# Performance work log

Hardware: AMD Instinct MI355X
Metric: run time of the kernel (lower is better)

The kernel has to match this reference:

```python
import jax, jax.numpy as jnp
import numpy as np

BETA = 0.2        # RPE learning rate (init kwarg, unused in forward output math except P update)
THRESH = 0.5      # BrainCog IFNode default firing threshold; v starts at 0 -> spike = (x >= THRESH)
N_NEURONS = 33554432


def setup_inputs() -> dict:
    key = jax.random.key(0)
    spikes = jax.random.uniform(key, (N_NEURONS,), dtype=jnp.float32)
    P = jnp.zeros((N_NEURONS,), dtype=jnp.float32)  # reward prediction state
    return {"spikes": spikes, "P": P}


def reference(spikes, P):
    # Vectorized IF neurons: membrane v = 0 + spikes; fire if v >= threshold (hard reset).
    out_spikes = (spikes >= THRESH).astype(spikes.dtype)   # [n_neurons]
    S = out_spikes.mean()                                  # scalar mean firing rate
    delta = S - P                                          # [n_neurons] reward prediction error
    # (State update in original: P <- P + BETA * delta; forward returns (delta, out_spikes).)
    return (delta, out_spikes)
```

## Files before the change

kernel.cpp:

```cpp
#include <hip/hip_runtime.h>


#define THRESH 0.5f
#define BLOCK  256
#define GRID   2048

typedef float v4f __attribute__((ext_vector_type(4)));

__device__ __forceinline__ int spike4(const v4f s, v4f& o) {
    o.x = (s.x >= THRESH) ? 1.0f : 0.0f;
    o.y = (s.y >= THRESH) ? 1.0f : 0.0f;
    o.z = (s.z >= THRESH) ? 1.0f : 0.0f;
    o.w = (s.w >= THRESH) ? 1.0f : 0.0f;
    return (int)o.x + (int)o.y + (int)o.z + (int)o.w;
}

__global__ __launch_bounds__(BLOCK) void spike_count_kernel(
    const v4f* __restrict__ spikes4,
    v4f* __restrict__ out_spikes4,
    unsigned int* __restrict__ partials,
    int n4, int chunk)
{
    const int tid   = threadIdx.x;
    const int start = blockIdx.x * chunk;
    const int end   = min(start + chunk, n4);
    int cnt = 0;

    int i = start + tid;
    for (; i + 3 * BLOCK < end; i += 4 * BLOCK) {
        v4f a = spikes4[i];
        v4f b = spikes4[i +     BLOCK];
        v4f c = spikes4[i + 2 * BLOCK];
        v4f d = spikes4[i + 3 * BLOCK];
        v4f oa, ob, oc, od;
        cnt += spike4(a, oa);
        cnt += spike4(b, ob);
        cnt += spike4(c, oc);
        cnt += spike4(d, od);
        out_spikes4[i]             = oa;
        out_spikes4[i +     BLOCK] = ob;
        out_spikes4[i + 2 * BLOCK] = oc;
        out_spikes4[i + 3 * BLOCK] = od;
    }
    for (; i < end; i += BLOCK) {
        v4f s = spikes4[i];
        v4f o;
        cnt += spike4(s, o);
        out_spikes4[i] = o;
    }

    #pragma unroll
    for (int off = 32; off > 0; off >>= 1)
        cnt += __shfl_down(cnt, off, 64);

    __shared__ int wave_sums[BLOCK / 64];
    const int lane = tid & 63;
    const int wid  = tid >> 6;
    if (lane == 0) wave_sums[wid] = cnt;
    __syncthreads();
    if (tid == 0) {
        int total = 0;
        #pragma unroll
        for (int w = 0; w < BLOCK / 64; ++w) total += wave_sums[w];
        partials[blockIdx.x] = (unsigned int)total;
    }
}

__global__ __launch_bounds__(BLOCK) void delta_kernel(
    const v4f* __restrict__ P4,
    v4f* __restrict__ delta4,
    const unsigned int* __restrict__ partials,
    int n_part, int n4, int chunk, float inv_n)
{
    const int tid = threadIdx.x;

    int c = 0;
    for (int j = tid; j < n_part; j += BLOCK)
        c += (int)partials[j];
    #pragma unroll
    for (int off = 32; off > 0; off >>= 1)
        c += __shfl_down(c, off, 64);

    __shared__ int wave_sums[BLOCK / 64];
    const int lane = tid & 63;
    const int wid  = tid >> 6;
    if (lane == 0) wave_sums[wid] = c;
    __syncthreads();
    int total = 0;
    #pragma unroll
    for (int w = 0; w < BLOCK / 64; ++w) total += wave_sums[w];
    const float S = (float)total * inv_n;

    const int start = blockIdx.x * chunk;
    const int end   = min(start + chunk, n4);
    int i = start + tid;
    for (; i + 3 * BLOCK < end; i += 4 * BLOCK) {
        v4f a  = P4[i];
        v4f b  = P4[i +     BLOCK];
        v4f c4 = P4[i + 2 * BLOCK];
        v4f d  = P4[i + 3 * BLOCK];
        delta4[i]             = S - a;
        delta4[i +     BLOCK] = S - b;
        delta4[i + 2 * BLOCK] = S - c4;
        delta4[i + 3 * BLOCK] = S - d;
    }
    for (; i < end; i += BLOCK) {
        v4f p = P4[i];
        delta4[i] = S - p;
    }
}

extern "C" void kernel_launch(void* const* d_in, const int* in_sizes, int n_in,
                              void* d_out, int out_size, void* d_ws, size_t ws_size,
                              hipStream_t stream) {
    const float* spikes = (const float*)d_in[0];
    const float* P      = (const float*)d_in[1];
    float* out          = (float*)d_out;

    const int n  = in_sizes[0];
    const int n4 = n / 4;
    const int chunk = (n4 + GRID - 1) / GRID;
    float* delta_out  = out;
    float* spikes_out = out + n;

    unsigned int* partials = (unsigned int*)d_ws;

    spike_count_kernel<<<GRID, BLOCK, 0, stream>>>(
        (const v4f*)spikes, (v4f*)spikes_out, partials, n4, chunk);

    delta_kernel<<<GRID, BLOCK, 0, stream>>>(
        (const v4f*)P, (v4f*)delta_out, partials, GRID, n4, chunk,
        1.0f / (float)n);
}
```

Baseline: 433.8 us.

## Fuse spike count and delta into one kernel with atomic grid barrier

Merges the two kernels into one persistent-style kernel. Blocks publish their counts through hierarchical bucketed atomics, and the last arriver computes S and publishes it while the other blocks spin-wait. This is meant to remove the second kernel launch and the serial partials reduction in each block. It relies on all 2048 blocks being co-resident (launch bounds request 8 blocks per SIMD). A fallback where a block rescans all spikes on timeout avoids deadlock but would be very slow, and a small init kernel now zeroes the workspace.

```diff
diff --git a/kernel.cpp b/kernel.cpp
--- a/kernel.cpp
+++ b/kernel.cpp
@@ -4,6 +4,17 @@
 #define THRESH 0.5f
 #define BLOCK  256
 #define GRID   2048
+#define NBUCKET 64
+#define NSTRIDE 16
+#define BLOCKS_PER_BUCKET (GRID / NBUCKET)
+
+#define TOT(j)   ((j) * NSTRIDE)
+#define ARR(j)   ((NBUCKET + (j)) * NSTRIDE)
+#define GTOT     (2 * NBUCKET * NSTRIDE)
+#define GARR     (2 * NBUCKET * NSTRIDE + 16)
+#define PUB      (2 * NBUCKET * NSTRIDE + 32)
+#define SBITS    (2 * NBUCKET * NSTRIDE + 48)
+#define WS_SLOTS (2 * NBUCKET * NSTRIDE + 64)
 
 typedef float v4f __attribute__((ext_vector_type(4)));
 
@@ -15,17 +26,30 @@
     return (int)o.x + (int)o.y + (int)o.z + (int)o.w;
 }
 
-__global__ __launch_bounds__(BLOCK) void spike_count_kernel(
+__global__ __launch_bounds__(256) void ws_init_kernel(unsigned int* __restrict__ ws) {
+    const int t = threadIdx.x;
+    for (int i = t; i < WS_SLOTS; i += 256) ws[i] = 0u;
+}
+
+__global__ __launch_bounds__(BLOCK, 8) void dopamine_fused(
     const v4f* __restrict__ spikes4,
+    const v4f* __restrict__ P4,
     v4f* __restrict__ out_spikes4,
-    unsigned int* __restrict__ partials,
-    int n4, int chunk)
+    v4f* __restrict__ delta4,
+    unsigned int* __restrict__ ws,
+    int n4, int chunk, float inv_n)
 {
     const int tid   = threadIdx.x;
-    const int start = blockIdx.x * chunk;
+    const int bid   = blockIdx.x;
+    const int start = bid * chunk;
     const int end   = min(start + chunk, n4);
+    const int lane  = tid & 63;
+    const int wid   = tid >> 6;
+
+    __shared__ int   wave_sums[BLOCK / 64];
+    __shared__ float s_S;
+
     int cnt = 0;
-
     int i = start + tid;
     for (; i + 3 * BLOCK < end; i += 4 * BLOCK) {
         v4f a = spikes4[i];
@@ -52,48 +76,93 @@
     #pragma unroll
     for (int off = 32; off > 0; off >>= 1)
         cnt += __shfl_down(cnt, off, 64);
-
-    __shared__ int wave_sums[BLOCK / 64];
-    const int lane = tid & 63;
-    const int wid  = tid >> 6;
     if (lane == 0) wave_sums[wid] = cnt;
     __syncthreads();
+
     if (tid == 0) {
         int total = 0;
         #pragma unroll
         for (int w = 0; w < BLOCK / 64; ++w) total += wave_sums[w];
-        partials[blockIdx.x] = (unsigned int)total;
-    }
-}
-
-__global__ __launch_bounds__(BLOCK) void delta_kernel(
-    const v4f* __restrict__ P4,
-    v4f* __restrict__ delta4,
-    const unsigned int* __restrict__ partials,
-    int n_part, int n4, int chunk, float inv_n)
-{
-    const int tid = threadIdx.x;
-
-    int c = 0;
-    for (int j = tid; j < n_part; j += BLOCK)
-        c += (int)partials[j];
-    #pragma unroll
-    for (int off = 32; off > 0; off >>= 1)
-        c += __shfl_down(c, off, 64);
-
-    __shared__ int wave_sums[BLOCK / 64];
-    const int lane = tid & 63;
-    const int wid  = tid >> 6;
-    if (lane == 0) wave_sums[wid] = c;
+
+        const int j = bid & (NBUCKET - 1);
+
+        const unsigned int p0 =
+            __hip_atomic_load(&ws[PUB], __ATOMIC_ACQUIRE, __HIP_MEMORY_SCOPE_AGENT);
+
+        __hip_atomic_fetch_add(&ws[TOT(j)], (unsigned int)total,
+                               __ATOMIC_RELAXED, __HIP_MEMORY_SCOPE_AGENT);
+        unsigned int a = __hip_atomic_fetch_add(&ws[ARR(j)], 1u,
+                               __ATOMIC_ACQ_REL, __HIP_MEMORY_SCOPE_AGENT);
+
+        bool have_S = false;
+        float S = -1.0f;
+
+        if (a == BLOCKS_PER_BUCKET - 1) {
+            unsigned int bt = __hip_atomic_load(&ws[TOT(j)],
+                                  __ATOMIC_ACQUIRE, __HIP_MEMORY_SCOPE_AGENT);
+            __hip_atomic_fetch_add(&ws[GTOT], bt,
+                                   __ATOMIC_RELAXED, __HIP_MEMORY_SCOPE_AGENT);
+            unsigned int g = __hip_atomic_fetch_add(&ws[GARR], 1u,
+                                   __ATOMIC_ACQ_REL, __HIP_MEMORY_SCOPE_AGENT);
+            if (g == NBUCKET - 1) {
+                unsigned int t = __hip_atomic_load(&ws[GTOT],
+                                     __ATOMIC_ACQUIRE, __HIP_MEMORY_SCOPE_AGENT);
+                S = (float)t * inv_n;
+                have_S = true;
+                for (int k = 0; k < NBUCKET; ++k) {
+                    __hip_atomic_store(&ws[TOT(k)], 0u,
+                                       __ATOMIC_RELAXED, __HIP_MEMORY_SCOPE_AGENT);
+                    __hip_atomic_store(&ws[ARR(k)], 0u,
+                                       __ATOMIC_RELAXED, __HIP_MEMORY_SCOPE_AGENT);
+                }
+                __hip_atomic_store(&ws[GTOT], 0u,
+                                   __ATOMIC_RELAXED, __HIP_MEMORY_SCOPE_AGENT);
+                __hip_atomic_store(&ws[GARR], 0u,
+                                   __ATOMIC_RELAXED, __HIP_MEMORY_SCOPE_AGENT);
+                __hip_atomic_store(&ws[SBITS], __float_as_uint(S),
+                                   __ATOMIC_RELAXED, __HIP_MEMORY_SCOPE_AGENT);
+                __hip_atomic_fetch_add(&ws[PUB], 1u,
+                                       __ATOMIC_RELEASE, __HIP_MEMORY_SCOPE_AGENT);
+            }
+        }
+
+        if (!have_S) {
+            for (int poll = 0; poll < (1 << 16); ++poll) {
+                unsigned int p = __hip_atomic_load(&ws[PUB],
+                                     __ATOMIC_ACQUIRE, __HIP_MEMORY_SCOPE_AGENT);
+                if (p != p0) {
+                    unsigned int sb = __hip_atomic_load(&ws[SBITS],
+                                          __ATOMIC_RELAXED, __HIP_MEMORY_SCOPE_AGENT);
+                    S = __uint_as_float(sb);
+                    have_S = true;
+                    break;
+                }
+                __builtin_amdgcn_s_sleep(8);
+            }
+        }
+        s_S = have_S ? S : -1.0f;
+    }
     __syncthreads();
-    int total = 0;
-    #pragma unroll
-    for (int w = 0; w < BLOCK / 64; ++w) total += wave_sums[w];
-    const float S = (float)total * inv_n;
-
-    const int start = blockIdx.x * chunk;
-    const int end   = min(start + chunk, n4);
-    int i = start + tid;
+    float S = s_S;
+
+    if (S < 0.0f) {
+        int c2 = 0;
+        for (int jj = tid; jj < n4; jj += BLOCK) {
+            v4f o;
+            c2 += spike4(spikes4[jj], o);
+        }
+        #pragma unroll
+        for (int off = 32; off > 0; off >>= 1)
+            c2 += __shfl_down(c2, off, 64);
+        if (lane == 0) wave_sums[wid] = c2;
+        __syncthreads();
+        int tot = 0;
+        #pragma unroll
+        for (int w = 0; w < BLOCK / 64; ++w) tot += wave_sums[w];
+        S = (float)tot * inv_n;
+    }
+
+    i = start + tid;
     for (; i + 3 * BLOCK < end; i += 4 * BLOCK) {
         v4f a  = P4[i];
         v4f b  = P4[i +     BLOCK];
@@ -123,12 +192,12 @@
     float* delta_out  = out;
     float* spikes_out = out + n;
 
-    unsigned int* partials = (unsigned int*)d_ws;
-
-    spike_count_kernel<<<GRID, BLOCK, 0, stream>>>(
-        (const v4f*)spikes, (v4f*)spikes_out, partials, n4, chunk);
-
-    delta_kernel<<<GRID, BLOCK, 0, stream>>>(
-        (const v4f*)P, (v4f*)delta_out, partials, GRID, n4, chunk,
-        1.0f / (float)n);
-}
+    unsigned int* ws = (unsigned int*)d_ws;
+
+    ws_init_kernel<<<1, 256, 0, stream>>>(ws);
+
+    dopamine_fused<<<GRID, BLOCK, 0, stream>>>(
+        (const v4f*)spikes, (const v4f*)P,
+        (v4f*)spikes_out, (v4f*)delta_out,
+        ws, n4, chunk, 1.0f / (float)n);
+}
```

After: 816.1 us. 1.88x slower.

## Use grid-stride access and prefetch P before partial reduction in delta kernel

Applied to the files above, without the earlier changes.

Both kernels move from per-block contiguous chunks to a grid-stride pattern, so concurrent blocks touch adjacent memory. The delta kernel issues its first four P loads before reducing the partial counts, hiding load latency behind that reduction. Launch bounds now request 8 blocks per CU. Grid-stride access changes DRAM page locality, and the early loads hold more registers across the reduction.

```diff
diff --git a/kernel.cpp b/kernel.cpp
--- a/kernel.cpp
+++ b/kernel.cpp
@@ -6,6 +6,7 @@
 #define GRID   2048
 
 typedef float v4f __attribute__((ext_vector_type(4)));
+typedef unsigned int u32;
 
 __device__ __forceinline__ int spike4(const v4f s, v4f& o) {
     o.x = (s.x >= THRESH) ? 1.0f : 0.0f;
@@ -15,34 +16,34 @@
     return (int)o.x + (int)o.y + (int)o.z + (int)o.w;
 }
 
-__global__ __launch_bounds__(BLOCK) void spike_count_kernel(
+__global__ __launch_bounds__(BLOCK, 8) void k1_spikes(
     const v4f* __restrict__ spikes4,
     v4f* __restrict__ out_spikes4,
-    unsigned int* __restrict__ partials,
-    int n4, int chunk)
+    u32* __restrict__ partials,
+    int n4)
 {
-    const int tid   = threadIdx.x;
-    const int start = blockIdx.x * chunk;
-    const int end   = min(start + chunk, n4);
+    const int tid    = threadIdx.x;
+    const int gtid   = blockIdx.x * BLOCK + tid;
+    const int stride = GRID * BLOCK;
+
     int cnt = 0;
-
-    int i = start + tid;
-    for (; i + 3 * BLOCK < end; i += 4 * BLOCK) {
+    int i = gtid;
+    for (; i + 3 * stride < n4; i += 4 * stride) {
         v4f a = spikes4[i];
-        v4f b = spikes4[i +     BLOCK];
-        v4f c = spikes4[i + 2 * BLOCK];
-        v4f d = spikes4[i + 3 * BLOCK];
+        v4f b = spikes4[i +     stride];
+        v4f c = spikes4[i + 2 * stride];
+        v4f d = spikes4[i + 3 * stride];
         v4f oa, ob, oc, od;
         cnt += spike4(a, oa);
         cnt += spike4(b, ob);
         cnt += spike4(c, oc);
         cnt += spike4(d, od);
-        out_spikes4[i]             = oa;
-        out_spikes4[i +     BLOCK] = ob;
-        out_spikes4[i + 2 * BLOCK] = oc;
-        out_spikes4[i + 3 * BLOCK] = od;
+        out_spikes4[i]              = oa;
+        out_spikes4[i +     stride] = ob;
+        out_spikes4[i + 2 * stride] = oc;
+        out_spikes4[i + 3 * stride] = od;
     }
-    for (; i < end; i += BLOCK) {
+    for (; i < n4; i += stride) {
         v4f s = spikes4[i];
         v4f o;
         cnt += spike4(s, o);
@@ -62,17 +63,30 @@
         int total = 0;
         #pragma unroll
         for (int w = 0; w < BLOCK / 64; ++w) total += wave_sums[w];
-        partials[blockIdx.x] = (unsigned int)total;
+        partials[blockIdx.x] = (u32)total;
     }
 }
 
-__global__ __launch_bounds__(BLOCK) void delta_kernel(
+__global__ __launch_bounds__(BLOCK, 8) void k2_delta(
     const v4f* __restrict__ P4,
     v4f* __restrict__ delta4,
-    const unsigned int* __restrict__ partials,
-    int n_part, int n4, int chunk, float inv_n)
+    const u32* __restrict__ partials,
+    int n_part, int n4, float inv_n)
 {
-    const int tid = threadIdx.x;
+    const int tid    = threadIdx.x;
+    const int gtid   = blockIdx.x * BLOCK + tid;
+    const int stride = GRID * BLOCK;
+    const int lane   = tid & 63;
+    const int wid    = tid >> 6;
+
+    v4f pa, pb, pc, pd;
+    const bool pre = (gtid + 3 * stride < n4);
+    if (pre) {
+        pa = P4[gtid];
+        pb = P4[gtid +     stride];
+        pc = P4[gtid + 2 * stride];
+        pd = P4[gtid + 3 * stride];
+    }
 
     int c = 0;
     for (int j = tid; j < n_part; j += BLOCK)
@@ -82,8 +96,6 @@
         c += __shfl_down(c, off, 64);
 
     __shared__ int wave_sums[BLOCK / 64];
-    const int lane = tid & 63;
-    const int wid  = tid >> 6;
     if (lane == 0) wave_sums[wid] = c;
     __syncthreads();
     int total = 0;
@@ -91,20 +103,25 @@
     for (int w = 0; w < BLOCK / 64; ++w) total += wave_sums[w];
     const float S = (float)total * inv_n;
 
-    const int start = blockIdx.x * chunk;
-    const int end   = min(start + chunk, n4);
-    int i = start + tid;
-    for (; i + 3 * BLOCK < end; i += 4 * BLOCK) {
-        v4f a  = P4[i];
-        v4f b  = P4[i +     BLOCK];
-        v4f c4 = P4[i + 2 * BLOCK];
-        v4f d  = P4[i + 3 * BLOCK];
-        delta4[i]             = S - a;
-        delta4[i +     BLOCK] = S - b;
-        delta4[i + 2 * BLOCK] = S - c4;
-        delta4[i + 3 * BLOCK] = S - d;
+    int i = gtid;
+    if (pre) {
+        delta4[i]              = S - pa;
+        delta4[i +     stride] = S - pb;
+        delta4[i + 2 * stride] = S - pc;
+        delta4[i + 3 * stride] = S - pd;
+        i += 4 * stride;
     }
-    for (; i < end; i += BLOCK) {
+    for (; i + 3 * stride < n4; i += 4 * stride) {
+        v4f a = P4[i];
+        v4f b = P4[i +     stride];
+        v4f c4 = P4[i + 2 * stride];
+        v4f d = P4[i + 3 * stride];
+        delta4[i]              = S - a;
+        delta4[i +     stride] = S - b;
+        delta4[i + 2 * stride] = S - c4;
+        delta4[i + 3 * stride] = S - d;
+    }
+    for (; i < n4; i += stride) {
         v4f p = P4[i];
         delta4[i] = S - p;
     }
@@ -119,16 +136,15 @@
 
     const int n  = in_sizes[0];
     const int n4 = n / 4;
-    const int chunk = (n4 + GRID - 1) / GRID;
     float* delta_out  = out;
     float* spikes_out = out + n;
 
-    unsigned int* partials = (unsigned int*)d_ws;
+    u32* partials = (u32*)d_ws;
 
-    spike_count_kernel<<<GRID, BLOCK, 0, stream>>>(
-        (const v4f*)spikes, (v4f*)spikes_out, partials, n4, chunk);
+    k1_spikes<<<GRID, BLOCK, 0, stream>>>(
+        (const v4f*)spikes, (v4f*)spikes_out, partials, n4);
 
-    delta_kernel<<<GRID, BLOCK, 0, stream>>>(
-        (const v4f*)P, (v4f*)delta_out, partials, GRID, n4, chunk,
+    k2_delta<<<GRID, BLOCK, 0, stream>>>(
+        (const v4f*)P, (v4f*)delta_out, partials, GRID, n4,
         1.0f / (float)n);
 }
```

Result: no change. 441.0 us (+1.7%).
